# Optimization experiments

Measured on AMD Instinct MI355X. Metric: run time of the kernel, lower is better.

## Reference

```python
import jax, jax.numpy as jnp
import numpy as np

E = 100000   # n_entities
R = 64       # n_relations
I = 256      # in_channels
O = 256      # out_channels
N_EDGES = 1_600_000


def setup_inputs() -> dict:
    key = jax.random.key(0)
    k1, k2, k3, k4 = jax.random.split(key, 4)
    x = jax.random.normal(k1, (E, I), dtype=jnp.float32)
    # cs must be nonzero (it is reciprocated); uniform in [0.5, 1.5)
    cs = jax.random.uniform(k2, (E, R), dtype=jnp.float32) + 0.5
    W = jax.random.normal(k3, (R, I, O), dtype=jnp.float32) * 0.05
    edge_index = jax.random.randint(k4, (2, N_EDGES), 0, E, dtype=jnp.int64)
    return {"x": x, "cs": cs, "W": W, "edge_index": edge_index}


def reference(x, cs, W, edge_index):
    # Faithful to: torch.einsum('er,rio,ej->eo', 1/cs, W, x)
    # i and j are independently contracted indices, so this factorizes:
    # out[e,o] = (sum_j x[e,j]) * sum_r (1/cs[e,r]) * (sum_i W[r,i,o])
    cs_reciprocal = 1.0 / cs                 # (E, R)
    W_sum = jnp.sum(W, axis=1)               # (R, O)
    x_sum = jnp.sum(x, axis=1)               # (E,)
    src = (cs_reciprocal @ W_sum) * x_sum[:, None]  # (E, O)
    return src
```

## Files before the change

### kernel.cpp

```cpp
#include <hip/hip_runtime.h>


constexpr int En = 100000;
constexpr int Rn = 64;
constexpr int In = 256;
constexpr int On = 256;
constexpr int TILES = En / 16;

constexpr int WSUM_BLOCKS = 256;
constexpr int XSUM_BLOCKS = 512;

typedef short bf16x8 __attribute__((ext_vector_type(8)));
typedef float floatx4 __attribute__((ext_vector_type(4)));

static __device__ __forceinline__ short f2bf(float f) {
    unsigned u = __builtin_bit_cast(unsigned, f);
    unsigned r = (u + 0x7FFFu + ((u >> 16) & 1u)) >> 16;
    return (short)r;
}

__global__ __launch_bounds__(1024) void pre_kernel(const float* __restrict__ W,
                                                   const float* __restrict__ x,
                                                   short* __restrict__ wsumT,
                                                   float* __restrict__ xsum,
                                                   int xstride) {
    __shared__ float red[16][65];
    if (blockIdx.x < WSUM_BLOCKS) {
        const int r  = blockIdx.x >> 2;
        const int h  = blockIdx.x & 3;
        const int ol = threadIdx.x & 63;
        const int ic = threadIdx.x >> 6;
        const int o  = h * 64 + ol;
        const float* base = W + ((size_t)r * In + (size_t)ic * 16) * On + o;
        float s = 0.f;
#pragma unroll
        for (int i = 0; i < 16; ++i) s += base[(size_t)i * On];
        red[ic][ol] = s;
        __syncthreads();
        if (ic == 0) {
            float t = 0.f;
#pragma unroll
            for (int j = 0; j < 16; ++j) t += red[j][ol];
            wsumT[o * Rn + r] = f2bf(t);
        }
    } else {
        const int w    = ((int)(blockIdx.x - WSUM_BLOCKS) * 1024 + (int)threadIdx.x) >> 6;
        const int nw   = (XSUM_BLOCKS * 1024) >> 6;
        const int lane = threadIdx.x & 63;
        for (int base = w * 4; base < En; base += nw * 4) {
            float s[4];
#pragma unroll
            for (int u = 0; u < 4; ++u) {
                const int row = base + u;
                float4 v = make_float4(0.f, 0.f, 0.f, 0.f);
                if (row < En)
                    v = *(const float4*)&x[(size_t)row * In + lane * 4];
                s[u] = (v.x + v.y) + (v.z + v.w);
            }
#pragma unroll
            for (int u = 0; u < 4; ++u) {
#pragma unroll
                for (int off = 32; off; off >>= 1) s[u] += __shfl_down(s[u], off, 64);
            }
            if (lane == 0) {
#pragma unroll
                for (int u = 0; u < 4; ++u)
                    if (base + u < En) xsum[(size_t)(base + u) * xstride] = s[u];
            }
        }
    }
}

__global__ __launch_bounds__(256, 4) void out_kernel(const float* __restrict__ cs,
                                                     const short* __restrict__ wsumT,
                                                     const float* __restrict__ xsum,
                                                     int xstride,
                                                     float* __restrict__ out) {
    const int gw = (blockIdx.x * 256 + (int)threadIdx.x) >> 6;
    if (gw >= TILES) return;
    const int ln = threadIdx.x & 63;
    const int lm = ln & 15;
    const int q  = ln >> 4;
    const int e0 = gw * 16 + lm;

    const float* p = cs + (size_t)e0 * Rn + q * 8;
    const float4 d0 = *(const float4*)p;
    const float4 d1 = *(const float4*)(p + 4);
    const float4 d2 = *(const float4*)(p + 32);
    const float4 d3 = *(const float4*)(p + 36);
    const float xs  = xsum[(size_t)e0 * xstride];

    bf16x8 b0, b1;
    {
        const float rv[16] = {d0.x, d0.y, d0.z, d0.w, d1.x, d1.y, d1.z, d1.w,
                              d2.x, d2.y, d2.z, d2.w, d3.x, d3.y, d3.z, d3.w};
#pragma unroll
        for (int j = 0; j < 8; ++j) {
            b0[j] = f2bf(__builtin_amdgcn_rcpf(rv[j]));
            b1[j] = f2bf(__builtin_amdgcn_rcpf(rv[8 + j]));
        }
    }

    float* orow = out + (size_t)e0 * On + q * 4;
    const short* wb = wsumT + lm * Rn + q * 8;
#pragma unroll
    for (int ot = 0; ot < 16; ++ot) {
        const short* wp = wb + ot * 16 * Rn;
        const bf16x8 wa0 = *(const bf16x8*)wp;
        const bf16x8 wa1 = *(const bf16x8*)(wp + 32);
        floatx4 acc = {0.f, 0.f, 0.f, 0.f};
        acc = __builtin_amdgcn_mfma_f32_16x16x32_bf16(wa0, b0, acc, 0, 0, 0);
        acc = __builtin_amdgcn_mfma_f32_16x16x32_bf16(wa1, b1, acc, 0, 0, 0);
        const float4 st = make_float4(acc[0] * xs, acc[1] * xs,
                                      acc[2] * xs, acc[3] * xs);
        *(float4*)(orow + ot * 16) = st;
    }
}

extern "C" void kernel_launch(void* const* d_in, const int* in_sizes, int n_in,
                              void* d_out, int out_size, void* d_ws, size_t ws_size,
                              hipStream_t stream) {
    const float* x  = (const float*)d_in[0];
    const float* cs = (const float*)d_in[1];
    const float* W  = (const float*)d_in[2];
    float* out = (float*)d_out;

    short* wsumT = (short*)d_ws;
    float* xsum;
    int xstride;
    if (ws_size >= (size_t)(32768 + En * 4)) {
        xsum = (float*)((char*)d_ws + 32768);
        xstride = 1;
    } else {
        xsum = out;
        xstride = On;
    }

    pre_kernel<<<dim3(WSUM_BLOCKS + XSUM_BLOCKS), dim3(1024), 0, stream>>>(
        W, x, wsumT, xsum, xstride);
    out_kernel<<<dim3((TILES * 64 + 255) / 256), dim3(256), 0, stream>>>(
        cs, wsumT, xsum, xstride, out);
}
```

Measured before the change: 243.3 us.

## Fuse x row-sum into output kernel and drop xsum intermediate

Moves the per-entity x row reduction out of the pre-pass into the MFMA output kernel. Each group of 16 lanes sums a 64-float slice of its row, then two xor-shuffles combine the four slices. This removes the xsum write and re-read and shrinks the first kernel to the W-sum work only. The cost is that the out kernel now carries the 102 MB x read, and its strided per-lane loads may coalesce less well than the old row-contiguous reads.

```diff
diff --git a/kernel.cpp b/kernel.cpp
--- a/kernel.cpp
+++ b/kernel.cpp
@@ -6,9 +6,6 @@
 constexpr int In = 256;
 constexpr int On = 256;
 constexpr int TILES = En / 16;
-
-constexpr int WSUM_BLOCKS = 256;
-constexpr int XSUM_BLOCKS = 512;
 
 typedef short bf16x8 __attribute__((ext_vector_type(8)));
 typedef float floatx4 __attribute__((ext_vector_type(4)));
@@ -19,62 +16,31 @@
     return (short)r;
 }
 
-__global__ __launch_bounds__(1024) void pre_kernel(const float* __restrict__ W,
-                                                   const float* __restrict__ x,
-                                                   short* __restrict__ wsumT,
-                                                   float* __restrict__ xsum,
-                                                   int xstride) {
+__global__ __launch_bounds__(1024) void wsum_kernel(const float* __restrict__ W,
+                                                    short* __restrict__ wsumT) {
     __shared__ float red[16][65];
-    if (blockIdx.x < WSUM_BLOCKS) {
-        const int r  = blockIdx.x >> 2;
-        const int h  = blockIdx.x & 3;
-        const int ol = threadIdx.x & 63;
-        const int ic = threadIdx.x >> 6;
-        const int o  = h * 64 + ol;
-        const float* base = W + ((size_t)r * In + (size_t)ic * 16) * On + o;
-        float s = 0.f;
+    const int r  = blockIdx.x >> 2;
+    const int h  = blockIdx.x & 3;
+    const int ol = threadIdx.x & 63;
+    const int ic = threadIdx.x >> 6;
+    const int o  = h * 64 + ol;
+    const float* base = W + ((size_t)r * In + (size_t)ic * 16) * On + o;
+    float s = 0.f;
 #pragma unroll
-        for (int i = 0; i < 16; ++i) s += base[(size_t)i * On];
-        red[ic][ol] = s;
-        __syncthreads();
-        if (ic == 0) {
-            float t = 0.f;
+    for (int i = 0; i < 16; ++i) s += base[(size_t)i * On];
+    red[ic][ol] = s;
+    __syncthreads();
+    if (ic == 0) {
+        float t = 0.f;
 #pragma unroll
-            for (int j = 0; j < 16; ++j) t += red[j][ol];
-            wsumT[o * Rn + r] = f2bf(t);
-        }
-    } else {
-        const int w    = ((int)(blockIdx.x - WSUM_BLOCKS) * 1024 + (int)threadIdx.x) >> 6;
-        const int nw   = (XSUM_BLOCKS * 1024) >> 6;
-        const int lane = threadIdx.x & 63;
-        for (int base = w * 4; base < En; base += nw * 4) {
-            float s[4];
-#pragma unroll
-            for (int u = 0; u < 4; ++u) {
-                const int row = base + u;
-                float4 v = make_float4(0.f, 0.f, 0.f, 0.f);
-                if (row < En)
-                    v = *(const float4*)&x[(size_t)row * In + lane * 4];
-                s[u] = (v.x + v.y) + (v.z + v.w);
-            }
-#pragma unroll
-            for (int u = 0; u < 4; ++u) {
-#pragma unroll
-                for (int off = 32; off; off >>= 1) s[u] += __shfl_down(s[u], off, 64);
-            }
-            if (lane == 0) {
-#pragma unroll
-                for (int u = 0; u < 4; ++u)
-                    if (base + u < En) xsum[(size_t)(base + u) * xstride] = s[u];
-            }
-        }
+        for (int j = 0; j < 16; ++j) t += red[j][ol];
+        wsumT[o * Rn + r] = f2bf(t);
     }
 }
 
-__global__ __launch_bounds__(256, 4) void out_kernel(const float* __restrict__ cs,
+__global__ __launch_bounds__(256, 4) void out_kernel(const float* __restrict__ x,
+                                                     const float* __restrict__ cs,
                                                      const short* __restrict__ wsumT,
-                                                     const float* __restrict__ xsum,
-                                                     int xstride,
                                                      float* __restrict__ out) {
     const int gw = (blockIdx.x * 256 + (int)threadIdx.x) >> 6;
     if (gw >= TILES) return;
@@ -83,13 +49,26 @@
     const int q  = ln >> 4;
     const int e0 = gw * 16 + lm;
 
+    const floatx4* xp = (const floatx4*)(x + (size_t)e0 * In + q * 64);
+    floatx4 a0 = {0.f, 0.f, 0.f, 0.f}, a1 = a0, a2 = a0, a3 = a0;
+#pragma unroll
+    for (int j = 0; j < 4; ++j) {
+        a0 += xp[4 * j + 0];
+        a1 += xp[4 * j + 1];
+        a2 += xp[4 * j + 2];
+        a3 += xp[4 * j + 3];
+    }
+    const floatx4 at = (a0 + a1) + (a2 + a3);
+    float s = (at[0] + at[1]) + (at[2] + at[3]);
+    s += __shfl_xor(s, 16, 64);
+    s += __shfl_xor(s, 32, 64);
+    const float xs = s;
+
     const float* p = cs + (size_t)e0 * Rn + q * 8;
     const float4 d0 = *(const float4*)p;
     const float4 d1 = *(const float4*)(p + 4);
     const float4 d2 = *(const float4*)(p + 32);
     const float4 d3 = *(const float4*)(p + 36);
-    const float xs  = xsum[(size_t)e0 * xstride];
-
     bf16x8 b0, b1;
     {
         const float rv[16] = {d0.x, d0.y, d0.z, d0.w, d1.x, d1.y, d1.z, d1.w,
@@ -126,18 +105,8 @@
     float* out = (float*)d_out;
 
     short* wsumT = (short*)d_ws;
-    float* xsum;
-    int xstride;
-    if (ws_size >= (size_t)(32768 + En * 4)) {
-        xsum = (float*)((char*)d_ws + 32768);
-        xstride = 1;
-    } else {
-        xsum = out;
-        xstride = On;
-    }
 
-    pre_kernel<<<dim3(WSUM_BLOCKS + XSUM_BLOCKS), dim3(1024), 0, stream>>>(
-        W, x, wsumT, xsum, xstride);
+    wsum_kernel<<<dim3(256), dim3(1024), 0, stream>>>(W, wsumT);
     out_kernel<<<dim3((TILES * 64 + 255) / 256), dim3(256), 0, stream>>>(
-        cs, wsumT, xsum, xstride, out);
+        x, cs, wsumT, out);
 }
```

Measured after the change: 247.7 us. No clear change (+1.8%).
